# Kernel tuning notes

Hardware: AMD Instinct MI355X
Metric: run time of the kernel (lower is better)

Reference implementation:

```python
import jax, jax.numpy as jnp
import numpy as np

HID, INP = 128, 320
C = HID + INP  # 448


def _fake_quant_w(w):
    # brevitas Int8WeightPerTensorFloat-style symmetric per-tensor fake quant (STE forward)
    scale = jnp.maximum(jnp.max(jnp.abs(w)), 1e-8) / 127.0
    q = jnp.clip(jnp.round(w / scale), -128, 127) * scale
    return w + jax.lax.stop_gradient(q - w)


def _dwconv(x, w, b):
    # depthwise 3x3, SAME padding; w: [C,1,3,3]
    y = jax.lax.conv_general_dilated(x, _fake_quant_w(w), (1, 1), 'SAME',
                                     dimension_numbers=('NCHW', 'OIHW', 'NCHW'),
                                     feature_group_count=x.shape[1])
    return y + b[None, :, None, None]


def _pwconv(x, w, b):
    # pointwise 1x1; w: [O,C,1,1]
    y = jax.lax.conv_general_dilated(x, _fake_quant_w(w), (1, 1), 'SAME',
                                     dimension_numbers=('NCHW', 'OIHW', 'NCHW'))
    return y + b[None, :, None, None]


def setup_inputs() -> dict:
    key = jax.random.key(0)
    ks = jax.random.split(key, 16)
    B, H, W = 8, 64, 128
    d = {
        'h': jax.random.normal(ks[0], (B, HID, H, W), jnp.float32),
        'x': jax.random.normal(ks[1], (B, INP, H, W), jnp.float32),
    }
    i = 2
    for g in ('z', 'r', 'q'):
        d[f'wd{g}'] = jax.random.normal(ks[i], (C, 1, 3, 3), jnp.float32) * 0.1; i += 1
        d[f'bd{g}'] = jax.random.normal(ks[i], (C,), jnp.float32) * 0.01; i += 1
        d[f'wp{g}'] = jax.random.normal(ks[i], (HID, C, 1, 1), jnp.float32) * 0.05; i += 1
        d[f'bp{g}'] = jax.random.normal(ks[i], (HID,), jnp.float32) * 0.01; i += 1
    return d


def reference(h, x, wdz, bdz, wpz, bpz, wdr, bdr, wpr, bpr, wdq, bdq, wpq, bpq):
    hx = jnp.concatenate([h, x], axis=1)  # [B, 448, H, W]
    z = jax.nn.sigmoid(_pwconv(_dwconv(hx, wdz, bdz), wpz, bpz))
    r = jax.nn.sigmoid(_pwconv(_dwconv(hx, wdr, bdr), wpr, bpr))
    rhx = jnp.concatenate([r * h, x], axis=1)
    q = jnp.tanh(_pwconv(_dwconv(rhx, wdq, bdq), wpq, bpq))
    return (1.0 - z) * h + z * q
```

## Files before the change

### kernel.cpp

```cpp
#include <hip/hip_runtime.h>
#include <hip/hip_bf16.h>

#define BB  8
#define HIDC 128
#define INPC 320
#define CC  448
#define HH  64
#define WWI 128
#define HW  8192
#define NT_PER_B 512
#define KG  56

using bf16   = __hip_bfloat16;
using bf16x8 = __attribute__((ext_vector_type(8))) __bf16;
using bf16x4 = __attribute__((ext_vector_type(4))) __bf16;
using bf16x2 = __attribute__((ext_vector_type(2))) __bf16;
using f32x4  = __attribute__((ext_vector_type(4))) float;
using f32x2  = __attribute__((ext_vector_type(2))) float;

__device__ __forceinline__ float b2f(bf16 v) { return __bfloat162float(v); }
__device__ __forceinline__ bf16  f2b(float v) { return __float2bfloat16(v); }

__device__ __forceinline__ void load2(const float* p, float& v0, float& v1) {
  f32x2 t = *reinterpret_cast<const f32x2*>(p);
  v0 = t[0]; v1 = t[1];
}
__device__ __forceinline__ void load2(const bf16* p, float& v0, float& v1) {
  bf16x2 t = *reinterpret_cast<const bf16x2*>(p);
  v0 = (float)t[0]; v1 = (float)t[1];
}

__global__ __launch_bounds__(256) void quant_kernel(
    const float* wdz, const float* wpz, const float* wdr, const float* wpr,
    const float* wdq, const float* wpq, float* qwd, bf16* qwp, float* scales)
{
  const float* src = nullptr; int n = 0; float* df = nullptr; bf16* db = nullptr;
  int sidx = -1;
  switch (blockIdx.x) {
    case 0: src = wdz; n = CC * 9;    df = qwd;                 break;
    case 1: src = wpz; n = HIDC * CC; db = qwp;                 sidx = 0; break;
    case 2: src = wdr; n = CC * 9;    df = qwd + 4096;          break;
    case 3: src = wpr; n = HIDC * CC; db = qwp + HIDC * CC;     sidx = 1; break;
    case 4: src = wdq; n = CC * 9;    df = qwd + 8192;          break;
    case 5: src = wpq; n = HIDC * CC; db = qwp + 2 * HIDC * CC; sidx = 2; break;
  }
  __shared__ float red[256];
  int tid = threadIdx.x;
  float m = 0.f;
  for (int i = tid * 4; i < n; i += 1024) {
    f32x4 v = *reinterpret_cast<const f32x4*>(src + i);
    m = fmaxf(m, fmaxf(fmaxf(fabsf(v[0]), fabsf(v[1])), fmaxf(fabsf(v[2]), fabsf(v[3]))));
  }
  red[tid] = m; __syncthreads();
  for (int s = 128; s > 0; s >>= 1) {
    if (tid < s) red[tid] = fmaxf(red[tid], red[tid + s]);
    __syncthreads();
  }
  float scale = fmaxf(red[0], 1e-8f) / 127.f;
  if (sidx >= 0 && tid == 0) scales[sidx] = scale;
  for (int i = tid * 4; i < n; i += 1024) {
    f32x4 v = *reinterpret_cast<const f32x4*>(src + i);
    float q[4];
#pragma unroll
    for (int j = 0; j < 4; j++) {
      float qq = rintf(v[j] / scale);
      q[j] = fminf(fmaxf(qq, -128.f), 127.f);
    }
    if (df) {
      f32x4 o; o[0] = q[0] * scale; o[1] = q[1] * scale; o[2] = q[2] * scale; o[3] = q[3] * scale;
      *reinterpret_cast<f32x4*>(df + i) = o;
    } else {
      bf16x4 o; o[0] = (__bf16)q[0]; o[1] = (__bf16)q[1]; o[2] = (__bf16)q[2]; o[3] = (__bf16)q[3];
      *reinterpret_cast<bf16x4*>(db + i) = o;
    }
  }
}

template <int NG, typename TH>
__global__ __launch_bounds__(256) void dwconv_kernel(
    const TH*    __restrict__ src_h,
    const float* __restrict__ src_x,
    const float* __restrict__ w0, const float* __restrict__ b0,
    const float* __restrict__ w1, const float* __restrict__ b1,
    bf16* __restrict__ out0, bf16* __restrict__ out1)
{
  int cg   = blockIdx.x;
  int b    = blockIdx.z;
  int lane = threadIdx.x & 63;
  int w    = threadIdx.x >> 6;
  int y    = blockIdx.y * 4 + w;
  int x0   = lane * 2;
  int c0   = cg * 8;
  bool in_h = (c0 < HIDC);
  const TH*    baseh = src_h + ((size_t)b * HIDC + c0) * HW;
  const float* basex = src_x + ((size_t)b * INPC + (c0 - HIDC)) * HW;

  int  yc[3]; bool vld[3];
#pragma unroll
  for (int d = 0; d < 3; d++) {
    int yy = y + d - 1;
    vld[d] = (unsigned)yy < (unsigned)HH;
    yc[d]  = vld[d] ? yy : (yy < 0 ? 0 : HH - 1);
  }

  float v[8][3][2];
#pragma unroll
  for (int i = 0; i < 8; i++) {
    const TH*    ph = baseh + (size_t)i * HW;
    const float* pf = basex + (size_t)i * HW;
#pragma unroll
    for (int d = 0; d < 3; d++) {
      if (in_h) load2(ph + yc[d] * WWI + x0, v[i][d][0], v[i][d][1]);
      else      load2(pf + yc[d] * WWI + x0, v[i][d][0], v[i][d][1]);
    }
  }

  float a0[2][8], a1[2][8];
#pragma unroll
  for (int i = 0; i < 8; i++) {
    int c = c0 + i;
    float s00 = 0.f, s01 = 0.f, s10 = 0.f, s11 = 0.f;
#pragma unroll
    for (int d = 0; d < 3; d++) {
      float v0 = v[i][d][0], v1 = v[i][d][1];
      if (!vld[d]) { v0 = 0.f; v1 = 0.f; }
      float vL = __shfl_up(v1, 1);
      if (lane == 0)  vL = 0.f;
      float vR = __shfl_down(v0, 1);
      if (lane == 63) vR = 0.f;
      int t = d * 3;
      float u0 = w0[c * 9 + t], u1 = w0[c * 9 + t + 1], u2 = w0[c * 9 + t + 2];
      s00 += vL * u0 + v0 * u1 + v1 * u2;
      s01 += v0 * u0 + v1 * u1 + vR * u2;
      if (NG == 2) {
        float q0 = w1[c * 9 + t], q1 = w1[c * 9 + t + 1], q2 = w1[c * 9 + t + 2];
        s10 += vL * q0 + v0 * q1 + v1 * q2;
        s11 += v0 * q0 + v1 * q1 + vR * q2;
      }
    }
    float bb0 = b0[c];
    a0[0][i] = s00 + bb0;
    a0[1][i] = s01 + bb0;
    if (NG == 2) {
      float bb1 = b1[c];
      a1[0][i] = s10 + bb1;
      a1[1][i] = s11 + bb1;
    }
  }

#pragma unroll
  for (int p = 0; p < 2; p++) {
    int px = x0 + p;
    size_t off = (((size_t)b * NT_PER_B + y * 8 + (px >> 4)) * KG + cg) * 128 + (px & 15) * 8;
    bf16x8 v0;
#pragma unroll
    for (int i = 0; i < 8; i++) v0[i] = (__bf16)a0[p][i];
    *reinterpret_cast<bf16x8*>(out0 + off) = v0;
    if (NG == 2) {
      bf16x8 v1;
#pragma unroll
      for (int i = 0; i < 8; i++) v1[i] = (__bf16)a1[p][i];
      *reinterpret_cast<bf16x8*>(out1 + off) = v1;
    }
  }
}

__device__ __forceinline__ void pw_gemm(const bf16* __restrict__ dbt,
                                        const bf16* __restrict__ wpm,
                                        int lane, f32x4 acc[2][4])
{
  int quad = lane >> 4;
  int lr   = lane & 15;
  const bf16* wp0 = wpm + (size_t)lr * CC + quad * 8;
  const bf16* bsrc = dbt + (size_t)lane * 8;
#pragma unroll
  for (int kk = 0; kk < 14; kk++) {
    bf16x8 a0 = *reinterpret_cast<const bf16x8*>(wp0 + kk * 32);
    bf16x8 a1 = *reinterpret_cast<const bf16x8*>(wp0 + 16 * CC + kk * 32);
#pragma unroll
    for (int nf = 0; nf < 4; nf++) {
      bf16x8 bfr = *reinterpret_cast<const bf16x8*>(bsrc + ((size_t)nf * KG + kk * 4) * 128);
      acc[0][nf] = __builtin_amdgcn_mfma_f32_16x16x32_bf16(a0, bfr, acc[0][nf], 0, 0, 0);
      acc[1][nf] = __builtin_amdgcn_mfma_f32_16x16x32_bf16(a1, bfr, acc[1][nf], 0, 0, 0);
    }
  }
}

__global__ __launch_bounds__(256) void pw_zr_kernel(
    const bf16*  __restrict__ dz,
    const bf16*  __restrict__ dr,
    const bf16*  __restrict__ qwp,
    const float* __restrict__ bpz, const float* __restrict__ bpr,
    const float* __restrict__ scales,
    const float* __restrict__ h,
    bf16* __restrict__ zout, bf16* __restrict__ rhout)
{
  int gate = blockIdx.z;
  const bf16*  dbuf = gate ? dr : dz;
  const bf16*  wp   = qwp + (size_t)gate * HIDC * CC;
  const float* bp   = gate ? bpr : bpz;
  float s = scales[gate];

  int b    = blockIdx.y;
  int n0   = blockIdx.x * 64;
  int nt0  = blockIdx.x * 4;
  int wave = threadIdx.x >> 6;
  int lane = threadIdx.x & 63;
  int quad = lane >> 4;
  int lr   = lane & 15;
  int m0   = wave * 32;
  f32x4 acc[2][4] = {};
  const bf16* dbt = dbuf + ((size_t)b * NT_PER_B + nt0) * (KG * 128);

  pw_gemm(dbt, wp + (size_t)m0 * CC, lane, acc);

#pragma unroll
  for (int mf = 0; mf < 2; mf++) {
#pragma unroll
    for (int r = 0; r < 4; r++) {
      int o = m0 + mf * 16 + quad * 4 + r;
      float bias = bp[o];
#pragma unroll
      for (int nf = 0; nf < 4; nf++) {
        int n = n0 + nf * 16 + lr;
        size_t idx = ((size_t)b * HIDC + o) * HW + n;
        float pre = acc[mf][nf][r] * s + bias;
        float sv  = 1.f / (1.f + expf(-pre));
        if (gate == 0) zout[idx]  = f2b(sv);
        else           rhout[idx] = f2b(sv * h[idx]);
      }
    }
  }
}

__global__ __launch_bounds__(256) void pw_q_kernel(
    const bf16*  __restrict__ dbuf,
    const bf16*  __restrict__ wp,
    const float* __restrict__ bp,
    const float* __restrict__ scale_p,
    const float* __restrict__ h,
    const bf16*  __restrict__ zin,
    float* __restrict__ qout)
{
  int b    = blockIdx.y;
  int n0   = blockIdx.x * 64;
  int nt0  = blockIdx.x * 4;
  int wave = threadIdx.x >> 6;
  int lane = threadIdx.x & 63;
  int quad = lane >> 4;
  int lr   = lane & 15;
  int m0   = wave * 32;
  float s = *scale_p;
  f32x4 acc[2][4] = {};
  const bf16* dbt = dbuf + ((size_t)b * NT_PER_B + nt0) * (KG * 128);

  pw_gemm(dbt, wp + (size_t)m0 * CC, lane, acc);

#pragma unroll
  for (int mf = 0; mf < 2; mf++) {
#pragma unroll
    for (int r = 0; r < 4; r++) {
      int o = m0 + mf * 16 + quad * 4 + r;
      float bias = bp[o];
#pragma unroll
      for (int nf = 0; nf < 4; nf++) {
        int n = n0 + nf * 16 + lr;
        size_t idx = ((size_t)b * HIDC + o) * HW + n;
        float pre = acc[mf][nf][r] * s + bias;
        float qv = tanhf(pre);
        float zv = b2f(zin[idx]);
        float hv = h[idx];
        qout[idx] = (1.f - zv) * hv + zv * qv;
      }
    }
  }
}

extern "C" void kernel_launch(void* const* d_in, const int* in_sizes, int n_in,
                              void* d_out, int out_size, void* d_ws, size_t ws_size,
                              hipStream_t stream)
{
  const float* h   = (const float*)d_in[0];
  const float* x   = (const float*)d_in[1];
  const float* wdz = (const float*)d_in[2];
  const float* bdz = (const float*)d_in[3];
  const float* wpz = (const float*)d_in[4];
  const float* bpz = (const float*)d_in[5];
  const float* wdr = (const float*)d_in[6];
  const float* bdr = (const float*)d_in[7];
  const float* wpr = (const float*)d_in[8];
  const float* bpr = (const float*)d_in[9];
  const float* wdq = (const float*)d_in[10];
  const float* bdq = (const float*)d_in[11];
  const float* wpq = (const float*)d_in[12];
  const float* bpq = (const float*)d_in[13];

  char* ws = (char*)d_ws;
  float* qwd    = (float*)ws;
  float* scales = qwd + 12288;
  bf16*  qwp    = (bf16*)(ws + 65536);
  const size_t DBUF_ELEMS = (size_t)BB * NT_PER_B * KG * 128;
  bf16*  dz   = (bf16*)(ws + (1 << 20));
  bf16*  dr   = dz + DBUF_ELEMS;
  bf16*  zbuf = dr + DBUF_ELEMS;
  bf16*  rh   = zbuf + (size_t)BB * HIDC * HW;

  quant_kernel<<<6, 256, 0, stream>>>(wdz, wpz, wdr, wpr, wdq, wpq, qwd, qwp, scales);

  dim3 dgrid(56, 16, 8);
  dwconv_kernel<2, float><<<dgrid, 256, 0, stream>>>(h, x, qwd, bdz, qwd + 4096, bdr, dz, dr);

  dim3 zrgrid(128, 8, 2);
  pw_zr_kernel<<<zrgrid, 256, 0, stream>>>(dz, dr, qwp, bpz, bpr, scales, h, zbuf, rh);

  dwconv_kernel<1, bf16><<<dgrid, 256, 0, stream>>>(rh, x, qwd + 8192, bdq, nullptr, nullptr,
                                                    dz, nullptr);

  dim3 pgrid(128, 8);
  pw_q_kernel<<<pgrid, 256, 0, stream>>>(dz, qwp + 2 * HIDC * CC, bpq, scales + 2, h, zbuf,
                                         (float*)d_out);
}
```

Measured before the change: 378.6 us.

## Move z-gate pointwise GEMM off the critical path by co-launching with second dwconv

Splits the fused z/r pointwise launch so only the r gate runs before the second depthwise conv. The z-gate pointwise work then shares one launch with the q-branch depthwise conv through a block-index split. This lets the independent z GEMM overlap with the memory-bound dwconv instead of delaying it. It needs a separate dq buffer so dz is not overwritten while being read, and it falls back to the old sequence when the workspace is too small.

```diff
diff --git a/kernel.cpp b/kernel.cpp
--- a/kernel.cpp
+++ b/kernel.cpp
@@ -77,18 +77,16 @@
 }
 
 template <int NG, typename TH>
-__global__ __launch_bounds__(256) void dwconv_kernel(
-    const TH*    __restrict__ src_h,
-    const float* __restrict__ src_x,
+__device__ __forceinline__ void dw_body(
+    int cg, int yq, int b,
+    const TH*    __restrict__ src_h, const float* __restrict__ src_x,
     const float* __restrict__ w0, const float* __restrict__ b0,
     const float* __restrict__ w1, const float* __restrict__ b1,
     bf16* __restrict__ out0, bf16* __restrict__ out1)
 {
-  int cg   = blockIdx.x;
-  int b    = blockIdx.z;
   int lane = threadIdx.x & 63;
   int w    = threadIdx.x >> 6;
-  int y    = blockIdx.y * 4 + w;
+  int y    = yq * 4 + w;
   int x0   = lane * 2;
   int c0   = cg * 8;
   bool in_h = (c0 < HIDC);
@@ -165,6 +163,17 @@
   }
 }
 
+template <int NG, typename TH>
+__global__ __launch_bounds__(256) void dwconv_kernel(
+    const TH* __restrict__ src_h, const float* __restrict__ src_x,
+    const float* __restrict__ w0, const float* __restrict__ b0,
+    const float* __restrict__ w1, const float* __restrict__ b1,
+    bf16* __restrict__ out0, bf16* __restrict__ out1)
+{
+  dw_body<NG, TH>(blockIdx.x, blockIdx.y, blockIdx.z, src_h, src_x,
+                  w0, b0, w1, b1, out0, out1);
+}
+
 __device__ __forceinline__ void pw_gemm(const bf16* __restrict__ dbt,
                                         const bf16* __restrict__ wpm,
                                         int lane, f32x4 acc[2][4])
@@ -186,65 +195,16 @@
   }
 }
 
-__global__ __launch_bounds__(256) void pw_zr_kernel(
-    const bf16*  __restrict__ dz,
-    const bf16*  __restrict__ dr,
-    const bf16*  __restrict__ qwp,
-    const float* __restrict__ bpz, const float* __restrict__ bpr,
-    const float* __restrict__ scales,
-    const float* __restrict__ h,
-    bf16* __restrict__ zout, bf16* __restrict__ rhout)
-{
-  int gate = blockIdx.z;
-  const bf16*  dbuf = gate ? dr : dz;
-  const bf16*  wp   = qwp + (size_t)gate * HIDC * CC;
-  const float* bp   = gate ? bpr : bpz;
-  float s = scales[gate];
-
-  int b    = blockIdx.y;
-  int n0   = blockIdx.x * 64;
-  int nt0  = blockIdx.x * 4;
-  int wave = threadIdx.x >> 6;
-  int lane = threadIdx.x & 63;
-  int quad = lane >> 4;
-  int lr   = lane & 15;
-  int m0   = wave * 32;
-  f32x4 acc[2][4] = {};
-  const bf16* dbt = dbuf + ((size_t)b * NT_PER_B + nt0) * (KG * 128);
-
-  pw_gemm(dbt, wp + (size_t)m0 * CC, lane, acc);
-
-#pragma unroll
-  for (int mf = 0; mf < 2; mf++) {
-#pragma unroll
-    for (int r = 0; r < 4; r++) {
-      int o = m0 + mf * 16 + quad * 4 + r;
-      float bias = bp[o];
-#pragma unroll
-      for (int nf = 0; nf < 4; nf++) {
-        int n = n0 + nf * 16 + lr;
-        size_t idx = ((size_t)b * HIDC + o) * HW + n;
-        float pre = acc[mf][nf][r] * s + bias;
-        float sv  = 1.f / (1.f + expf(-pre));
-        if (gate == 0) zout[idx]  = f2b(sv);
-        else           rhout[idx] = f2b(sv * h[idx]);
-      }
-    }
-  }
-}
-
-__global__ __launch_bounds__(256) void pw_q_kernel(
-    const bf16*  __restrict__ dbuf,
-    const bf16*  __restrict__ wp,
-    const float* __restrict__ bp,
-    const float* __restrict__ scale_p,
-    const float* __restrict__ h,
-    const bf16*  __restrict__ zin,
-    float* __restrict__ qout)
-{
-  int b    = blockIdx.y;
-  int n0   = blockIdx.x * 64;
-  int nt0  = blockIdx.x * 4;
+template <int GATE>
+__device__ __forceinline__ void pw_body(
+    int ntile, int b,
+    const bf16*  __restrict__ dbuf, const bf16* __restrict__ wp,
+    const float* __restrict__ bp,   const float* __restrict__ scale_p,
+    const float* __restrict__ h,    const bf16* __restrict__ zin,
+    bf16* __restrict__ zout, bf16* __restrict__ rhout, float* __restrict__ qout)
+{
+  int n0   = ntile * 64;
+  int nt0  = ntile * 4;
   int wave = threadIdx.x >> 6;
   int lane = threadIdx.x & 63;
   int quad = lane >> 4;
@@ -267,12 +227,51 @@
         int n = n0 + nf * 16 + lr;
         size_t idx = ((size_t)b * HIDC + o) * HW + n;
         float pre = acc[mf][nf][r] * s + bias;
-        float qv = tanhf(pre);
-        float zv = b2f(zin[idx]);
-        float hv = h[idx];
-        qout[idx] = (1.f - zv) * hv + zv * qv;
+        if (GATE == 0) {
+          zout[idx] = f2b(1.f / (1.f + expf(-pre)));
+        } else if (GATE == 1) {
+          float rv = 1.f / (1.f + expf(-pre));
+          rhout[idx] = f2b(rv * h[idx]);
+        } else {
+          float qv = tanhf(pre);
+          float zv = b2f(zin[idx]);
+          float hv = h[idx];
+          qout[idx] = (1.f - zv) * hv + zv * qv;
+        }
       }
     }
+  }
+}
+
+template <int GATE>
+__global__ __launch_bounds__(256) void pw_kernel(
+    const bf16*  __restrict__ dbuf, const bf16* __restrict__ wp,
+    const float* __restrict__ bp,   const float* __restrict__ scale_p,
+    const float* __restrict__ h,    const bf16* __restrict__ zin,
+    bf16* __restrict__ zout, bf16* __restrict__ rhout, float* __restrict__ qout)
+{
+  pw_body<GATE>(blockIdx.x, blockIdx.y, dbuf, wp, bp, scale_p, h, zin,
+                zout, rhout, qout);
+}
+
+__global__ __launch_bounds__(256) void dw2_pwz_kernel(
+    const bf16*  __restrict__ rh,   const float* __restrict__ x,
+    const float* __restrict__ wdq,  const float* __restrict__ bdq,
+    bf16* __restrict__ dq,
+    const bf16*  __restrict__ dz,   const bf16* __restrict__ wpz,
+    const float* __restrict__ bpz,  const float* __restrict__ scale_z,
+    bf16* __restrict__ zout)
+{
+  int bid = blockIdx.x;
+  if (bid < 56 * 16 * 8) {
+    int cg = bid % 56;
+    int rem = bid / 56;
+    dw_body<1, bf16>(cg, rem % 16, rem / 16, rh, x, wdq, bdq, nullptr, nullptr,
+                     dq, nullptr);
+  } else {
+    int pb = bid - 56 * 16 * 8;
+    pw_body<0>(pb & 127, pb >> 7, dz, wpz, bpz, scale_z, nullptr, nullptr,
+               zout, nullptr, nullptr);
   }
 }
 
@@ -300,23 +299,39 @@
   float* scales = qwd + 12288;
   bf16*  qwp    = (bf16*)(ws + 65536);
   const size_t DBUF_ELEMS = (size_t)BB * NT_PER_B * KG * 128;
+  const size_t ZB_ELEMS   = (size_t)BB * HIDC * HW;
   bf16*  dz   = (bf16*)(ws + (1 << 20));
   bf16*  dr   = dz + DBUF_ELEMS;
   bf16*  zbuf = dr + DBUF_ELEMS;
-  bf16*  rh   = zbuf + (size_t)BB * HIDC * HW;
+  bf16*  rh   = zbuf + ZB_ELEMS;
+  bf16*  dq   = rh + ZB_ELEMS;
+  const size_t NEED = (1 << 20) + (3 * DBUF_ELEMS + 2 * ZB_ELEMS) * sizeof(bf16);
 
   quant_kernel<<<6, 256, 0, stream>>>(wdz, wpz, wdr, wpr, wdq, wpq, qwd, qwp, scales);
 
   dim3 dgrid(56, 16, 8);
   dwconv_kernel<2, float><<<dgrid, 256, 0, stream>>>(h, x, qwd, bdz, qwd + 4096, bdr, dz, dr);
 
-  dim3 zrgrid(128, 8, 2);
-  pw_zr_kernel<<<zrgrid, 256, 0, stream>>>(dz, dr, qwp, bpz, bpr, scales, h, zbuf, rh);
-
-  dwconv_kernel<1, bf16><<<dgrid, 256, 0, stream>>>(rh, x, qwd + 8192, bdq, nullptr, nullptr,
-                                                    dz, nullptr);
-
   dim3 pgrid(128, 8);
-  pw_q_kernel<<<pgrid, 256, 0, stream>>>(dz, qwp + 2 * HIDC * CC, bpq, scales + 2, h, zbuf,
-                                         (float*)d_out);
-}
+
+  if (ws_size >= NEED) {
+    pw_kernel<1><<<pgrid, 256, 0, stream>>>(dr, qwp + HIDC * CC, bpr, scales + 1,
+                                            h, nullptr, nullptr, rh, nullptr);
+
+    dw2_pwz_kernel<<<56 * 16 * 8 + 128 * 8, 256, 0, stream>>>(
+        rh, x, qwd + 8192, bdq, dq,
+        dz, qwp, bpz, scales + 0, zbuf);
+
+    pw_kernel<2><<<pgrid, 256, 0, stream>>>(dq, qwp + 2 * HIDC * CC, bpq, scales + 2,
+                                            h, zbuf, nullptr, nullptr, (float*)d_out);
+  } else {
+    pw_kernel<0><<<pgrid, 256, 0, stream>>>(dz, qwp, bpz, scales + 0,
+                                            nullptr, nullptr, zbuf, nullptr, nullptr);
+    pw_kernel<1><<<pgrid, 256, 0, stream>>>(dr, qwp + HIDC * CC, bpr, scales + 1,
+                                            h, nullptr, nullptr, rh, nullptr);
+    dwconv_kernel<1, bf16><<<dgrid, 256, 0, stream>>>(rh, x, qwd + 8192, bdq,
+                                                      nullptr, nullptr, dz, nullptr);
+    pw_kernel<2><<<pgrid, 256, 0, stream>>>(dz, qwp + 2 * HIDC * CC, bpq, scales + 2,
+                                            h, zbuf, nullptr, nullptr, (float*)d_out);
+  }
+}
```

After: 410.7 us. 8.5% more time.
